# Optimization experiments

Measured on AMD Instinct MI355X. Metric: run time of the kernel, lower is better.

Reference implementation:

```python
import jax, jax.numpy as jnp
import numpy as np

N = 100000          # number of nodes (nums)
E = 1200000         # nnz of the normalized adjacency
D = 64              # embed_size; layer_size = [64, 64, 64]
NODE_DROP = 0.1     # args.node_dropout[0]
MESS_DROP = (0.1, 0.1, 0.1)
EPS = 1e-12         # F.normalize eps


def setup_inputs() -> dict:
    key = jax.random.key(0)
    ks = jax.random.split(key, 10)
    rows = jax.random.randint(ks[0], (E,), 0, N, dtype=jnp.int32)
    cols = jax.random.randint(ks[1], (E,), 0, N, dtype=jnp.int32)
    vals = jax.random.uniform(ks[2], (E,), dtype=jnp.float32)
    emb = jax.random.normal(ks[3], (N, D), dtype=jnp.float32) * 0.1
    W0 = jax.random.normal(ks[4], (D, D), dtype=jnp.float32) * 0.1
    b0 = jax.random.normal(ks[5], (1, D), dtype=jnp.float32) * 0.1
    W1 = jax.random.normal(ks[6], (D, D), dtype=jnp.float32) * 0.1
    b1 = jax.random.normal(ks[7], (1, D), dtype=jnp.float32) * 0.1
    W2 = jax.random.normal(ks[8], (D, D), dtype=jnp.float32) * 0.1
    b2 = jax.random.normal(ks[9], (1, D), dtype=jnp.float32) * 0.1
    return dict(rows=rows, cols=cols, vals=vals, emb=emb,
                W0=W0, b0=b0, W1=W1, b1=b1, W2=W2, b2=b2)


def reference(rows, cols, vals, emb, W0, b0, W1, b1, W2, b2):
    drop_key = jax.random.key(42)
    k_node, k0, k1, k2 = jax.random.split(drop_key, 4)

    # sparse node dropout: zero dropped edge values (== removing nnz), scale survivors
    keep_e = jax.random.bernoulli(k_node, 1.0 - NODE_DROP, (E,))
    a_vals = jnp.where(keep_e, vals / (1.0 - NODE_DROP), 0.0)

    def layer(ego, W, b, rate, k):
        # SpMM: out[r] += a_vals * ego[c]   (COO scatter-add)
        side = jax.ops.segment_sum(a_vals[:, None] * ego[cols], rows, num_segments=N)
        h = side @ W + b
        keep = jax.random.bernoulli(k, 1.0 - rate, h.shape)
        h = jnp.where(keep, h / (1.0 - rate), 0.0)          # mess dropout
        nrm = h / jnp.maximum(jnp.linalg.norm(h, axis=1, keepdims=True), EPS)
        return h, nrm  # ego continues as the (un-normalized) dropped output

    all_embs = [emb]
    ego = emb
    for (W, b, rate, k) in ((W0, b0, MESS_DROP[0], k0),
                            (W1, b1, MESS_DROP[1], k1),
                            (W2, b2, MESS_DROP[2], k2)):
        ego, nrm = layer(ego, W, b, rate, k)
        all_embs.append(nrm)
    return jnp.concatenate(all_embs, axis=1)  # [N, 4*D]
```

## Files before the change

kernel.cpp:

```cpp
#include <hip/hip_runtime.h>
#include <stdint.h>

#define N_NODES 100000
#define DIM 64
#define E_EDGES 1200000
#define RPB 16
#define NB 6250
#define BCAP 264
#define ROW_CAP 40
#define BPB 16

__host__ __device__ __forceinline__ void tf2x32(uint32_t k0, uint32_t k1,
                                                uint32_t c0, uint32_t c1,
                                                uint32_t& o0, uint32_t& o1) {
    uint32_t ks2 = k0 ^ k1 ^ 0x1BD11BDAu;
    uint32_t x0 = c0 + k0, x1 = c1 + k1;
#define TF_RND(r) { x0 += x1; x1 = (x1 << r) | (x1 >> (32 - r)); x1 ^= x0; }
    TF_RND(13) TF_RND(15) TF_RND(26) TF_RND(6)
    x0 += k1;  x1 += ks2 + 1u;
    TF_RND(17) TF_RND(29) TF_RND(16) TF_RND(24)
    x0 += ks2; x1 += k0 + 2u;
    TF_RND(13) TF_RND(15) TF_RND(26) TF_RND(6)
    x0 += k0;  x1 += k1 + 3u;
    TF_RND(17) TF_RND(29) TF_RND(16) TF_RND(24)
    x0 += k1;  x1 += ks2 + 4u;
    TF_RND(13) TF_RND(15) TF_RND(26) TF_RND(6)
    x0 += ks2; x1 += k0 + 5u;
#undef TF_RND
    o0 = x0; o1 = x1;
}

__device__ __forceinline__ bool keep_bit(uint32_t k0, uint32_t k1, uint32_t idx) {
    uint32_t y0, y1;
    tf2x32(k0, k1, 0u, idx, y0, y1);
    return (((y0 ^ y1) >> 9) < 7549747u);
}

__device__ __forceinline__ uint16_t f2bf(float f) {
    uint32_t x = __float_as_uint(f);
    return (uint16_t)((x + 0x7fffu + ((x >> 16) & 1u)) >> 16);
}

__global__ void k_bucket(const int* __restrict__ rows, const int* __restrict__ cols,
                         const float* __restrict__ vals, int* __restrict__ bcnt,
                         int2* __restrict__ bedge, uint32_t k0, uint32_t k1) {
    int i = blockIdx.x * blockDim.x + threadIdx.x;
    int stride = gridDim.x * blockDim.x;
    for (; i < E_EDGES; i += stride) {
        if (keep_bit(k0, k1, (uint32_t)i)) {
            int r = rows[i];
            int b = r >> 4;
            int rl = r & (RPB - 1);
            int pos = atomicAdd(&bcnt[b], 1);
            if (pos < BCAP)
                bedge[(size_t)b * BCAP + pos] =
                    make_int2((rl << 17) | cols[i],
                              __float_as_int(vals[i] * (1.0f / 0.9f)));
        }
    }
}

__global__ __launch_bounds__(256) void k_bin(const int2* __restrict__ bedge,
                                             const int* __restrict__ bcnt,
                                             uint32_t* __restrict__ pairs,
                                             int* __restrict__ cnt) {
    __shared__ uint32_t lp[256 * ROW_CAP];
    __shared__ int lc[256];
    int blk = blockIdx.x, t = threadIdx.x;
    for (int i = t; i < 256 * ROW_CAP / 4; i += 256)
        ((uint4*)lp)[i] = make_uint4(0u, 0u, 0u, 0u);
    lc[t] = 0;
    __syncthreads();
    int b0 = blk * BPB;
    int nb = NB - b0; if (nb > BPB) nb = BPB;
    for (int lb = 0; lb < nb; ++lb) {
        int bb = b0 + lb;
        int ne = bcnt[bb];
        if (ne > BCAP) ne = BCAP;
        const int2* be = bedge + (size_t)bb * BCAP;
        for (int e = t; e < ne; e += 256) {
            int2 en = be[e];
            uint32_t meta = (uint32_t)en.x;
            int rl = (int)(meta >> 17);
            uint32_t col = meta & 0x1FFFFu;
            float v = __int_as_float(en.y);
            int rloc = lb * RPB + rl;
            int pos = atomicAdd(&lc[rloc], 1);
            if (pos < ROW_CAP) {
                uint32_t q = (uint32_t)(v * 16384.0f + 0.5f);
                lp[rloc * ROW_CAP + pos] = (q << 17) | col;
            }
        }
    }
    __syncthreads();
    int nrows = N_NODES - blk * 256;
    if (nrows > 256) nrows = 256;
    int nq = nrows * ROW_CAP / 4;
    uint4* dst = (uint4*)(pairs + (size_t)blk * 256 * ROW_CAP);
    const uint4* src = (const uint4*)lp;
    for (int i = t; i < nq; i += 256) dst[i] = src[i];
    if (t < nrows) cnt[blk * 256 + t] = lc[t];
}

__global__ void k_embcvt(const float* __restrict__ emb, float* __restrict__ out,
                         uint16_t* __restrict__ egoA) {
    int i = blockIdx.x * blockDim.x + threadIdx.x;
    int stride = gridDim.x * blockDim.x;
    const int total = N_NODES * 16;
    for (; i < total; i += stride) {
        int n = i >> 4, q = i & 15;
        float4 v = ((const float4*)emb)[(size_t)n * 16 + q];
        ((float4*)out)[(size_t)n * 64 + q] = v;
        ushort4 bb;
        bb.x = f2bf(v.x); bb.y = f2bf(v.y); bb.z = f2bf(v.z); bb.w = f2bf(v.w);
        ((ushort4*)egoA)[(size_t)n * 16 + q] = bb;
    }
}

#define GATHER_FMA(V, aE, aO)                                              \
    {                                                                      \
        uint32_t c0 = V.x & 0x1FFFFu;  float a0 = (float)(V.x >> 17) * S;  \
        uint32_t c1 = V.y & 0x1FFFFu;  float a1 = (float)(V.y >> 17) * S;  \
        uint32_t c2 = V.z & 0x1FFFFu;  float a2 = (float)(V.z >> 17) * S;  \
        uint32_t c3 = V.w & 0x1FFFFu;  float a3 = (float)(V.w >> 17) * S;  \
        uint32_t u0 = egoU[c0 * 32u + (uint32_t)l2];                       \
        uint32_t u1 = egoU[c1 * 32u + (uint32_t)l2];                       \
        uint32_t u2 = egoU[c2 * 32u + (uint32_t)l2];                       \
        uint32_t u3 = egoU[c3 * 32u + (uint32_t)l2];                       \
        aE = fmaf(a0, __uint_as_float(u0 << 16), aE);                      \
        aO = fmaf(a0, __uint_as_float(u0 & 0xffff0000u), aO);              \
        aE = fmaf(a1, __uint_as_float(u1 << 16), aE);                      \
        aO = fmaf(a1, __uint_as_float(u1 & 0xffff0000u), aO);              \
        aE = fmaf(a2, __uint_as_float(u2 << 16), aE);                      \
        aO = fmaf(a2, __uint_as_float(u2 & 0xffff0000u), aO);              \
        aE = fmaf(a3, __uint_as_float(u3 << 16), aE);                      \
        aO = fmaf(a3, __uint_as_float(u3 & 0xffff0000u), aO);              \
    }

__global__ __launch_bounds__(256, 4) void k_layer(
    const int* __restrict__ cnt, const uint32_t* __restrict__ pairs,
    const uint16_t* __restrict__ ego_in,
    uint16_t* __restrict__ h_out,
    float* __restrict__ out, int coloff,
    const float* __restrict__ W, const float* __restrict__ bias,
    uint32_t k0, uint32_t k1) {
    __shared__ float sS[8][64];
    int t = threadIdx.x;
    int w = t >> 6, lane = t & 63;

    float wreg[64];
#pragma unroll
    for (int k = 0; k < 64; ++k)
        wreg[k] = W[k * 64 + lane];
    float breg = bias[lane];

    const float S = 1.0f / 16384.0f;
    int l2 = lane & 31;
    int hi4 = (lane >> 5) << 2;
    const uint32_t* egoU = (const uint32_t*)ego_in;
    int wid0 = blockIdx.x * 4 + w;
    const int NW = 2048 * 4;
    const int NPAIR = N_NODES / 2;
    for (int nn = wid0; nn < NPAIR; nn += NW) {
        int un0 = __builtin_amdgcn_readfirstlane(nn * 2);
        int un1 = un0 + 1;
        int len0 = (cnt[un0] + 7) & ~7;  if (len0 > ROW_CAP) len0 = ROW_CAP;
        int len1 = (cnt[un1] + 7) & ~7;  if (len1 > ROW_CAP) len1 = ROW_CAP;
        const uint32_t* rowp0 = pairs + (size_t)un0 * ROW_CAP + hi4;
        const uint32_t* rowp1 = pairs + (size_t)un1 * ROW_CAP + hi4;
        float accE0 = 0.f, accO0 = 0.f, accE1 = 0.f, accO1 = 0.f;
        int jmax = len0 > len1 ? len0 : len1;
        for (int j = 0; j < jmax; j += 8) {
            uint4 V0 = (j < len0) ? *reinterpret_cast<const uint4*>(rowp0 + j)
                                  : make_uint4(0u, 0u, 0u, 0u);
            uint4 V1 = (j < len1) ? *reinterpret_cast<const uint4*>(rowp1 + j)
                                  : make_uint4(0u, 0u, 0u, 0u);
            GATHER_FMA(V0, accE0, accO0)
            GATHER_FMA(V1, accE1, accO1)
        }
        accE0 += __shfl_xor(accE0, 32, 64);
        accO0 += __shfl_xor(accO0, 32, 64);
        accE1 += __shfl_xor(accE1, 32, 64);
        accO1 += __shfl_xor(accO1, 32, 64);
        if (lane < 32) {
            reinterpret_cast<float2*>(&sS[2 * w][0])[l2] = make_float2(accE0, accO0);
            reinterpret_cast<float2*>(&sS[2 * w + 1][0])[l2] = make_float2(accE1, accO1);
        }
        float h0 = breg, h1 = breg;
        const float4* s4p0 = reinterpret_cast<const float4*>(&sS[2 * w][0]);
        const float4* s4p1 = reinterpret_cast<const float4*>(&sS[2 * w + 1][0]);
#pragma unroll
        for (int kq = 0; kq < 16; ++kq) {
            float4 s40 = s4p0[kq];
            float4 s41 = s4p1[kq];
            h0 = fmaf(s40.x, wreg[4 * kq + 0], h0);
            h1 = fmaf(s41.x, wreg[4 * kq + 0], h1);
            h0 = fmaf(s40.y, wreg[4 * kq + 1], h0);
            h1 = fmaf(s41.y, wreg[4 * kq + 1], h1);
            h0 = fmaf(s40.z, wreg[4 * kq + 2], h0);
            h1 = fmaf(s41.z, wreg[4 * kq + 2], h1);
            h0 = fmaf(s40.w, wreg[4 * kq + 3], h0);
            h1 = fmaf(s41.w, wreg[4 * kq + 3], h1);
        }
        h0 = keep_bit(k0, k1, (uint32_t)un0 * 64u + (uint32_t)lane) ? h0 * (1.0f / 0.9f) : 0.0f;
        h1 = keep_bit(k0, k1, (uint32_t)un1 * 64u + (uint32_t)lane) ? h1 * (1.0f / 0.9f) : 0.0f;
        float s0 = h0 * h0, s1 = h1 * h1;
#pragma unroll
        for (int o = 32; o > 0; o >>= 1) {
            s0 += __shfl_xor(s0, o, 64);
            s1 += __shfl_xor(s1, o, 64);
        }
        float nv0 = h0 / fmaxf(sqrtf(s0), 1e-12f);
        float nv1 = h1 / fmaxf(sqrtf(s1), 1e-12f);
        if (h_out) {
            h_out[(size_t)un0 * DIM + lane] = f2bf(h0);
            h_out[(size_t)un1 * DIM + lane] = f2bf(h1);
        }
        out[(size_t)un0 * 256 + coloff + lane] = nv0;
        out[(size_t)un1 * 256 + coloff + lane] = nv1;
    }
}

extern "C" void kernel_launch(void* const* d_in, const int* in_sizes, int n_in,
                              void* d_out, int out_size, void* d_ws, size_t ws_size,
                              hipStream_t stream) {
    const int*   rows = (const int*)d_in[0];
    const int*   cols = (const int*)d_in[1];
    const float* vals = (const float*)d_in[2];
    const float* emb  = (const float*)d_in[3];
    const float* Wk[3] = { (const float*)d_in[4], (const float*)d_in[6], (const float*)d_in[8] };
    const float* bk[3] = { (const float*)d_in[5], (const float*)d_in[7], (const float*)d_in[9] };
    float* out = (float*)d_out;

    int*      bcnt  = (int*)d_ws;
    int*      cnt   = bcnt + 8192;
    int2*     bedge = (int2*)((char*)d_ws + 32768 + 400000);
    uint32_t* pairs = (uint32_t*)(bedge + (size_t)NB * BCAP);
    uint16_t* egoA  = (uint16_t*)(pairs + (size_t)N_NODES * ROW_CAP);
    uint16_t* egoB  = egoA + (size_t)N_NODES * DIM;

    uint32_t kn[2], kl[3][2];
    tf2x32(0u, 42u, 0u, 0u, kn[0], kn[1]);
    tf2x32(0u, 42u, 0u, 1u, kl[0][0], kl[0][1]);
    tf2x32(0u, 42u, 0u, 2u, kl[1][0], kl[1][1]);
    tf2x32(0u, 42u, 0u, 3u, kl[2][0], kl[2][1]);

    hipMemsetAsync(bcnt, 0, 8192 * 4, stream);
    k_bucket<<<2048, 256, 0, stream>>>(rows, cols, vals, bcnt, bedge, kn[0], kn[1]);
    k_bin<<<(NB + BPB - 1) / BPB, 256, 0, stream>>>(bedge, bcnt, pairs, cnt);
    k_embcvt<<<2048, 256, 0, stream>>>(emb, out, egoA);

    k_layer<<<2048, 256, 0, stream>>>(cnt, pairs, egoA, egoB, out, 64,
                                      Wk[0], bk[0], kl[0][0], kl[0][1]);
    k_layer<<<2048, 256, 0, stream>>>(cnt, pairs, egoB, egoA, out, 128,
                                      Wk[1], bk[1], kl[1][0], kl[1][1]);
    k_layer<<<2048, 256, 0, stream>>>(cnt, pairs, egoA, nullptr, out, 192,
                                      Wk[2], bk[2], kl[2][0], kl[2][1]);
}
```

Measured before the change: 237.5 us.

## Replicate bucket counters, fuse counter reset into embcvt, process four rows per wave

Bucket counters are replicated 8 ways by block index to reduce atomic contention in k_bucket, and k_bin consumes the replicas with one wave per cell. The memset is folded into k_embcvt, which now runs first. k_layer handles four rows per wave instead of two, giving more gather loads in flight, with launch bounds lowered to 3 blocks per SM. The risks are lower occupancy, per-replica overflow at 64 entries silently dropping edges, and more padded iterations when row lengths differ.

```diff
diff --git a/kernel.cpp b/kernel.cpp
--- a/kernel.cpp
+++ b/kernel.cpp
@@ -4,9 +4,9 @@
 #define N_NODES 100000
 #define DIM 64
 #define E_EDGES 1200000
-#define RPB 16
-#define NB 6250
-#define BCAP 264
+#define NBK 6250
+#define NREP 8
+#define BCAP_R 64
 #define ROW_CAP 40
 #define BPB 16
 
@@ -41,19 +41,37 @@
     return (uint16_t)((x + 0x7fffu + ((x >> 16) & 1u)) >> 16);
 }
 
+__global__ void k_embcvt(const float* __restrict__ emb, float* __restrict__ out,
+                         uint16_t* __restrict__ egoA, int* __restrict__ bcnt) {
+    int gid = blockIdx.x * blockDim.x + threadIdx.x;
+    if (gid < NREP * NBK) bcnt[gid] = 0;
+    int stride = gridDim.x * blockDim.x;
+    const int total = N_NODES * 16;
+    for (int i = gid; i < total; i += stride) {
+        int n = i >> 4, q = i & 15;
+        float4 v = ((const float4*)emb)[(size_t)n * 16 + q];
+        ((float4*)out)[(size_t)n * 64 + q] = v;
+        ushort4 bb;
+        bb.x = f2bf(v.x); bb.y = f2bf(v.y); bb.z = f2bf(v.z); bb.w = f2bf(v.w);
+        ((ushort4*)egoA)[(size_t)n * 16 + q] = bb;
+    }
+}
+
 __global__ void k_bucket(const int* __restrict__ rows, const int* __restrict__ cols,
                          const float* __restrict__ vals, int* __restrict__ bcnt,
                          int2* __restrict__ bedge, uint32_t k0, uint32_t k1) {
+    int rep = blockIdx.x & (NREP - 1);
     int i = blockIdx.x * blockDim.x + threadIdx.x;
     int stride = gridDim.x * blockDim.x;
     for (; i < E_EDGES; i += stride) {
         if (keep_bit(k0, k1, (uint32_t)i)) {
             int r = rows[i];
             int b = r >> 4;
-            int rl = r & (RPB - 1);
-            int pos = atomicAdd(&bcnt[b], 1);
-            if (pos < BCAP)
-                bedge[(size_t)b * BCAP + pos] =
+            int rl = r & 15;
+            int cell = rep * NBK + b;
+            int pos = atomicAdd(&bcnt[cell], 1);
+            if (pos < BCAP_R)
+                bedge[(size_t)cell * BCAP_R + pos] =
                     make_int2((rl << 17) | cols[i],
                               __float_as_int(vals[i] * (1.0f / 0.9f)));
         }
@@ -66,25 +84,30 @@
                                              int* __restrict__ cnt) {
     __shared__ uint32_t lp[256 * ROW_CAP];
     __shared__ int lc[256];
+    __shared__ int lcc[BPB * NREP];
     int blk = blockIdx.x, t = threadIdx.x;
     for (int i = t; i < 256 * ROW_CAP / 4; i += 256)
         ((uint4*)lp)[i] = make_uint4(0u, 0u, 0u, 0u);
     lc[t] = 0;
+    int b0 = blk * BPB;
+    if (t < BPB * NREP) {
+        int lb = t >> 3, rep = t & 7;
+        int ne = bcnt[rep * NBK + b0 + lb];
+        lcc[t] = (ne > BCAP_R) ? BCAP_R : ne;
+    }
     __syncthreads();
-    int b0 = blk * BPB;
-    int nb = NB - b0; if (nb > BPB) nb = BPB;
-    for (int lb = 0; lb < nb; ++lb) {
-        int bb = b0 + lb;
-        int ne = bcnt[bb];
-        if (ne > BCAP) ne = BCAP;
-        const int2* be = bedge + (size_t)bb * BCAP;
-        for (int e = t; e < ne; e += 256) {
-            int2 en = be[e];
+    int e = t & 63, wv = t >> 6;
+    for (int cc = 0; cc < BPB * NREP; cc += 4) {
+        int cell = cc + wv;
+        int lb = cell >> 3, rep = cell & 7;
+        int ne = lcc[cell];
+        if (e < ne) {
+            int2 en = bedge[((size_t)(rep * NBK + b0 + lb)) * BCAP_R + e];
             uint32_t meta = (uint32_t)en.x;
             int rl = (int)(meta >> 17);
             uint32_t col = meta & 0x1FFFFu;
             float v = __int_as_float(en.y);
-            int rloc = lb * RPB + rl;
+            int rloc = lb * 16 + rl;
             int pos = atomicAdd(&lc[rloc], 1);
             if (pos < ROW_CAP) {
                 uint32_t q = (uint32_t)(v * 16384.0f + 0.5f);
@@ -100,21 +123,6 @@
     const uint4* src = (const uint4*)lp;
     for (int i = t; i < nq; i += 256) dst[i] = src[i];
     if (t < nrows) cnt[blk * 256 + t] = lc[t];
-}
-
-__global__ void k_embcvt(const float* __restrict__ emb, float* __restrict__ out,
-                         uint16_t* __restrict__ egoA) {
-    int i = blockIdx.x * blockDim.x + threadIdx.x;
-    int stride = gridDim.x * blockDim.x;
-    const int total = N_NODES * 16;
-    for (; i < total; i += stride) {
-        int n = i >> 4, q = i & 15;
-        float4 v = ((const float4*)emb)[(size_t)n * 16 + q];
-        ((float4*)out)[(size_t)n * 64 + q] = v;
-        ushort4 bb;
-        bb.x = f2bf(v.x); bb.y = f2bf(v.y); bb.z = f2bf(v.z); bb.w = f2bf(v.w);
-        ((ushort4*)egoA)[(size_t)n * 16 + q] = bb;
-    }
 }
 
 #define GATHER_FMA(V, aE, aO)                                              \
@@ -137,14 +145,14 @@
         aO = fmaf(a3, __uint_as_float(u3 & 0xffff0000u), aO);              \
     }
 
-__global__ __launch_bounds__(256, 4) void k_layer(
+__global__ __launch_bounds__(256, 3) void k_layer(
     const int* __restrict__ cnt, const uint32_t* __restrict__ pairs,
     const uint16_t* __restrict__ ego_in,
     uint16_t* __restrict__ h_out,
     float* __restrict__ out, int coloff,
     const float* __restrict__ W, const float* __restrict__ bias,
     uint32_t k0, uint32_t k1) {
-    __shared__ float sS[8][64];
+    __shared__ float sS[16][64];
     int t = threadIdx.x;
     int w = t >> 6, lane = t & 63;
 
@@ -156,68 +164,90 @@
 
     const float S = 1.0f / 16384.0f;
     int l2 = lane & 31;
-    int hi4 = (lane >> 5) << 2;
+    int hiSel = lane >> 5;
+    int hi4 = hiSel << 2;
     const uint32_t* egoU = (const uint32_t*)ego_in;
     int wid0 = blockIdx.x * 4 + w;
     const int NW = 2048 * 4;
-    const int NPAIR = N_NODES / 2;
-    for (int nn = wid0; nn < NPAIR; nn += NW) {
-        int un0 = __builtin_amdgcn_readfirstlane(nn * 2);
-        int un1 = un0 + 1;
-        int len0 = (cnt[un0] + 7) & ~7;  if (len0 > ROW_CAP) len0 = ROW_CAP;
-        int len1 = (cnt[un1] + 7) & ~7;  if (len1 > ROW_CAP) len1 = ROW_CAP;
-        const uint32_t* rowp0 = pairs + (size_t)un0 * ROW_CAP + hi4;
-        const uint32_t* rowp1 = pairs + (size_t)un1 * ROW_CAP + hi4;
-        float accE0 = 0.f, accO0 = 0.f, accE1 = 0.f, accO1 = 0.f;
-        int jmax = len0 > len1 ? len0 : len1;
+    const int NQ = N_NODES / 4;
+    for (int q = wid0; q < NQ; q += NW) {
+        int un = __builtin_amdgcn_readfirstlane(q * 4);
+        int len0 = (cnt[un + 0] + 7) & ~7;  if (len0 > ROW_CAP) len0 = ROW_CAP;
+        int len1 = (cnt[un + 1] + 7) & ~7;  if (len1 > ROW_CAP) len1 = ROW_CAP;
+        int len2 = (cnt[un + 2] + 7) & ~7;  if (len2 > ROW_CAP) len2 = ROW_CAP;
+        int len3 = (cnt[un + 3] + 7) & ~7;  if (len3 > ROW_CAP) len3 = ROW_CAP;
+        const uint32_t* rp = pairs + (size_t)un * ROW_CAP + hi4;
+        float aE0 = 0.f, aO0 = 0.f, aE1 = 0.f, aO1 = 0.f;
+        float aE2 = 0.f, aO2 = 0.f, aE3 = 0.f, aO3 = 0.f;
+        int jmax = len0;
+        if (len1 > jmax) jmax = len1;
+        if (len2 > jmax) jmax = len2;
+        if (len3 > jmax) jmax = len3;
+        const uint4 zed = make_uint4(0u, 0u, 0u, 0u);
         for (int j = 0; j < jmax; j += 8) {
-            uint4 V0 = (j < len0) ? *reinterpret_cast<const uint4*>(rowp0 + j)
-                                  : make_uint4(0u, 0u, 0u, 0u);
-            uint4 V1 = (j < len1) ? *reinterpret_cast<const uint4*>(rowp1 + j)
-                                  : make_uint4(0u, 0u, 0u, 0u);
-            GATHER_FMA(V0, accE0, accO0)
-            GATHER_FMA(V1, accE1, accO1)
-        }
-        accE0 += __shfl_xor(accE0, 32, 64);
-        accO0 += __shfl_xor(accO0, 32, 64);
-        accE1 += __shfl_xor(accE1, 32, 64);
-        accO1 += __shfl_xor(accO1, 32, 64);
-        if (lane < 32) {
-            reinterpret_cast<float2*>(&sS[2 * w][0])[l2] = make_float2(accE0, accO0);
-            reinterpret_cast<float2*>(&sS[2 * w + 1][0])[l2] = make_float2(accE1, accO1);
-        }
-        float h0 = breg, h1 = breg;
-        const float4* s4p0 = reinterpret_cast<const float4*>(&sS[2 * w][0]);
-        const float4* s4p1 = reinterpret_cast<const float4*>(&sS[2 * w + 1][0]);
+            uint4 V0 = (j < len0) ? *reinterpret_cast<const uint4*>(rp + j) : zed;
+            uint4 V1 = (j < len1) ? *reinterpret_cast<const uint4*>(rp + ROW_CAP + j) : zed;
+            uint4 V2 = (j < len2) ? *reinterpret_cast<const uint4*>(rp + 2 * ROW_CAP + j) : zed;
+            uint4 V3 = (j < len3) ? *reinterpret_cast<const uint4*>(rp + 3 * ROW_CAP + j) : zed;
+            GATHER_FMA(V0, aE0, aO0)
+            GATHER_FMA(V1, aE1, aO1)
+            GATHER_FMA(V2, aE2, aO2)
+            GATHER_FMA(V3, aE3, aO3)
+        }
+        aE0 += __shfl_xor(aE0, 32, 64);  aO0 += __shfl_xor(aO0, 32, 64);
+        aE1 += __shfl_xor(aE1, 32, 64);  aO1 += __shfl_xor(aO1, 32, 64);
+        aE2 += __shfl_xor(aE2, 32, 64);  aO2 += __shfl_xor(aO2, 32, 64);
+        aE3 += __shfl_xor(aE3, 32, 64);  aO3 += __shfl_xor(aO3, 32, 64);
+        float2 vA = hiSel ? make_float2(aE2, aO2) : make_float2(aE0, aO0);
+        float2 vB = hiSel ? make_float2(aE3, aO3) : make_float2(aE1, aO1);
+        reinterpret_cast<float2*>(&sS[4 * w + 2 * hiSel][0])[l2] = vA;
+        reinterpret_cast<float2*>(&sS[4 * w + 2 * hiSel + 1][0])[l2] = vB;
+        float h0 = breg, h1 = breg, h2 = breg, h3 = breg;
+        const float4* s0p = reinterpret_cast<const float4*>(&sS[4 * w + 0][0]);
+        const float4* s1p = reinterpret_cast<const float4*>(&sS[4 * w + 1][0]);
+        const float4* s2p = reinterpret_cast<const float4*>(&sS[4 * w + 2][0]);
+        const float4* s3p = reinterpret_cast<const float4*>(&sS[4 * w + 3][0]);
 #pragma unroll
         for (int kq = 0; kq < 16; ++kq) {
-            float4 s40 = s4p0[kq];
-            float4 s41 = s4p1[kq];
-            h0 = fmaf(s40.x, wreg[4 * kq + 0], h0);
-            h1 = fmaf(s41.x, wreg[4 * kq + 0], h1);
-            h0 = fmaf(s40.y, wreg[4 * kq + 1], h0);
-            h1 = fmaf(s41.y, wreg[4 * kq + 1], h1);
-            h0 = fmaf(s40.z, wreg[4 * kq + 2], h0);
-            h1 = fmaf(s41.z, wreg[4 * kq + 2], h1);
-            h0 = fmaf(s40.w, wreg[4 * kq + 3], h0);
-            h1 = fmaf(s41.w, wreg[4 * kq + 3], h1);
-        }
-        h0 = keep_bit(k0, k1, (uint32_t)un0 * 64u + (uint32_t)lane) ? h0 * (1.0f / 0.9f) : 0.0f;
-        h1 = keep_bit(k0, k1, (uint32_t)un1 * 64u + (uint32_t)lane) ? h1 * (1.0f / 0.9f) : 0.0f;
-        float s0 = h0 * h0, s1 = h1 * h1;
+            float4 s0 = s0p[kq], s1 = s1p[kq], s2 = s2p[kq], s3 = s3p[kq];
+            float w0 = wreg[4 * kq + 0], w1 = wreg[4 * kq + 1];
+            float w2 = wreg[4 * kq + 2], w3 = wreg[4 * kq + 3];
+            h0 = fmaf(s0.x, w0, h0); h1 = fmaf(s1.x, w0, h1);
+            h2 = fmaf(s2.x, w0, h2); h3 = fmaf(s3.x, w0, h3);
+            h0 = fmaf(s0.y, w1, h0); h1 = fmaf(s1.y, w1, h1);
+            h2 = fmaf(s2.y, w1, h2); h3 = fmaf(s3.y, w1, h3);
+            h0 = fmaf(s0.z, w2, h0); h1 = fmaf(s1.z, w2, h1);
+            h2 = fmaf(s2.z, w2, h2); h3 = fmaf(s3.z, w2, h3);
+            h0 = fmaf(s0.w, w3, h0); h1 = fmaf(s1.w, w3, h1);
+            h2 = fmaf(s2.w, w3, h2); h3 = fmaf(s3.w, w3, h3);
+        }
+        uint32_t base_idx = (uint32_t)un * 64u + (uint32_t)lane;
+        h0 = keep_bit(k0, k1, base_idx)        ? h0 * (1.0f / 0.9f) : 0.0f;
+        h1 = keep_bit(k0, k1, base_idx + 64u)  ? h1 * (1.0f / 0.9f) : 0.0f;
+        h2 = keep_bit(k0, k1, base_idx + 128u) ? h2 * (1.0f / 0.9f) : 0.0f;
+        h3 = keep_bit(k0, k1, base_idx + 192u) ? h3 * (1.0f / 0.9f) : 0.0f;
+        float s0 = h0 * h0, s1 = h1 * h1, s2 = h2 * h2, s3 = h3 * h3;
 #pragma unroll
         for (int o = 32; o > 0; o >>= 1) {
             s0 += __shfl_xor(s0, o, 64);
             s1 += __shfl_xor(s1, o, 64);
+            s2 += __shfl_xor(s2, o, 64);
+            s3 += __shfl_xor(s3, o, 64);
         }
         float nv0 = h0 / fmaxf(sqrtf(s0), 1e-12f);
         float nv1 = h1 / fmaxf(sqrtf(s1), 1e-12f);
+        float nv2 = h2 / fmaxf(sqrtf(s2), 1e-12f);
+        float nv3 = h3 / fmaxf(sqrtf(s3), 1e-12f);
         if (h_out) {
-            h_out[(size_t)un0 * DIM + lane] = f2bf(h0);
-            h_out[(size_t)un1 * DIM + lane] = f2bf(h1);
-        }
-        out[(size_t)un0 * 256 + coloff + lane] = nv0;
-        out[(size_t)un1 * 256 + coloff + lane] = nv1;
+            h_out[(size_t)(un + 0) * DIM + lane] = f2bf(h0);
+            h_out[(size_t)(un + 1) * DIM + lane] = f2bf(h1);
+            h_out[(size_t)(un + 2) * DIM + lane] = f2bf(h2);
+            h_out[(size_t)(un + 3) * DIM + lane] = f2bf(h3);
+        }
+        out[(size_t)(un + 0) * 256 + coloff + lane] = nv0;
+        out[(size_t)(un + 1) * 256 + coloff + lane] = nv1;
+        out[(size_t)(un + 2) * 256 + coloff + lane] = nv2;
+        out[(size_t)(un + 3) * 256 + coloff + lane] = nv3;
     }
 }
 
@@ -233,9 +263,10 @@
     float* out = (float*)d_out;
 
     int*      bcnt  = (int*)d_ws;
-    int*      cnt   = bcnt + 8192;
-    int2*     bedge = (int2*)((char*)d_ws + 32768 + 400000);
-    uint32_t* pairs = (uint32_t*)(bedge + (size_t)NB * BCAP);
+    int*      cnt   = bcnt + 65536;
+    int2*     bedge = (int2*)(cnt + 100000 + 14);
+    bedge = (int2*)(((uintptr_t)bedge + 511) & ~(uintptr_t)511);
+    uint32_t* pairs = (uint32_t*)(bedge + (size_t)NREP * NBK * BCAP_R);
     uint16_t* egoA  = (uint16_t*)(pairs + (size_t)N_NODES * ROW_CAP);
     uint16_t* egoB  = egoA + (size_t)N_NODES * DIM;
 
@@ -245,10 +276,9 @@
     tf2x32(0u, 42u, 0u, 2u, kl[1][0], kl[1][1]);
     tf2x32(0u, 42u, 0u, 3u, kl[2][0], kl[2][1]);
 
-    hipMemsetAsync(bcnt, 0, 8192 * 4, stream);
+    k_embcvt<<<2048, 256, 0, stream>>>(emb, out, egoA, bcnt);
     k_bucket<<<2048, 256, 0, stream>>>(rows, cols, vals, bcnt, bedge, kn[0], kn[1]);
-    k_bin<<<(NB + BPB - 1) / BPB, 256, 0, stream>>>(bedge, bcnt, pairs, cnt);
-    k_embcvt<<<2048, 256, 0, stream>>>(emb, out, egoA);
+    k_bin<<<(NBK + BPB - 1) / BPB, 256, 0, stream>>>(bedge, bcnt, pairs, cnt);
 
     k_layer<<<2048, 256, 0, stream>>>(cnt, pairs, egoA, egoB, out, 64,
                                       Wk[0], bk[0], kl[0][0], kl[0][1]);
```

Result: slower. 257.5 us (+8.4%).

## Replicate bucket counters by block to cut atomic contention; fold memset into embcvt

Applied to the files above, without the earlier changes.

The COO bucketing now keeps eight replica bucket arrays, one per block-index modulo eight. This spreads the global atomicAdd contention on each bucket counter across replicas, and each replica has a smaller capacity. The binning kernel reads all replicas, one wavefront per cell, to build the per-row lists. The hipMemsetAsync that cleared the counters is removed and the clearing is folded into the embedding-convert kernel, which now runs first. The trade-off is more workspace, many mostly-empty 64-slot cells read in k_bin, and a new risk that a replica cell overflows its 64-entry cap.

```diff
diff --git a/kernel.cpp b/kernel.cpp
--- a/kernel.cpp
+++ b/kernel.cpp
@@ -4,9 +4,9 @@
 #define N_NODES 100000
 #define DIM 64
 #define E_EDGES 1200000
-#define RPB 16
-#define NB 6250
-#define BCAP 264
+#define NBK 6250
+#define NREP 8
+#define BCAP_R 64
 #define ROW_CAP 40
 #define BPB 16
 
@@ -41,19 +41,37 @@
     return (uint16_t)((x + 0x7fffu + ((x >> 16) & 1u)) >> 16);
 }
 
+__global__ void k_embcvt(const float* __restrict__ emb, float* __restrict__ out,
+                         uint16_t* __restrict__ egoA, int* __restrict__ bcnt) {
+    int gid = blockIdx.x * blockDim.x + threadIdx.x;
+    if (gid < NREP * NBK) bcnt[gid] = 0;
+    int stride = gridDim.x * blockDim.x;
+    const int total = N_NODES * 16;
+    for (int i = gid; i < total; i += stride) {
+        int n = i >> 4, q = i & 15;
+        float4 v = ((const float4*)emb)[(size_t)n * 16 + q];
+        ((float4*)out)[(size_t)n * 64 + q] = v;
+        ushort4 bb;
+        bb.x = f2bf(v.x); bb.y = f2bf(v.y); bb.z = f2bf(v.z); bb.w = f2bf(v.w);
+        ((ushort4*)egoA)[(size_t)n * 16 + q] = bb;
+    }
+}
+
 __global__ void k_bucket(const int* __restrict__ rows, const int* __restrict__ cols,
                          const float* __restrict__ vals, int* __restrict__ bcnt,
                          int2* __restrict__ bedge, uint32_t k0, uint32_t k1) {
+    int rep = blockIdx.x & (NREP - 1);
     int i = blockIdx.x * blockDim.x + threadIdx.x;
     int stride = gridDim.x * blockDim.x;
     for (; i < E_EDGES; i += stride) {
         if (keep_bit(k0, k1, (uint32_t)i)) {
             int r = rows[i];
             int b = r >> 4;
-            int rl = r & (RPB - 1);
-            int pos = atomicAdd(&bcnt[b], 1);
-            if (pos < BCAP)
-                bedge[(size_t)b * BCAP + pos] =
+            int rl = r & 15;
+            int cell = rep * NBK + b;
+            int pos = atomicAdd(&bcnt[cell], 1);
+            if (pos < BCAP_R)
+                bedge[(size_t)cell * BCAP_R + pos] =
                     make_int2((rl << 17) | cols[i],
                               __float_as_int(vals[i] * (1.0f / 0.9f)));
         }
@@ -66,25 +84,30 @@
                                              int* __restrict__ cnt) {
     __shared__ uint32_t lp[256 * ROW_CAP];
     __shared__ int lc[256];
+    __shared__ int lcc[BPB * NREP];
     int blk = blockIdx.x, t = threadIdx.x;
     for (int i = t; i < 256 * ROW_CAP / 4; i += 256)
         ((uint4*)lp)[i] = make_uint4(0u, 0u, 0u, 0u);
     lc[t] = 0;
+    int b0 = blk * BPB;
+    if (t < BPB * NREP) {
+        int lb = t >> 3, rep = t & 7;
+        int ne = bcnt[rep * NBK + b0 + lb];
+        lcc[t] = (ne > BCAP_R) ? BCAP_R : ne;
+    }
     __syncthreads();
-    int b0 = blk * BPB;
-    int nb = NB - b0; if (nb > BPB) nb = BPB;
-    for (int lb = 0; lb < nb; ++lb) {
-        int bb = b0 + lb;
-        int ne = bcnt[bb];
-        if (ne > BCAP) ne = BCAP;
-        const int2* be = bedge + (size_t)bb * BCAP;
-        for (int e = t; e < ne; e += 256) {
-            int2 en = be[e];
+    int e = t & 63, wv = t >> 6;
+    for (int cc = 0; cc < BPB * NREP; cc += 4) {
+        int cell = cc + wv;
+        int lb = cell >> 3, rep = cell & 7;
+        int ne = lcc[cell];
+        if (e < ne) {
+            int2 en = bedge[((size_t)(rep * NBK + b0 + lb)) * BCAP_R + e];
             uint32_t meta = (uint32_t)en.x;
             int rl = (int)(meta >> 17);
             uint32_t col = meta & 0x1FFFFu;
             float v = __int_as_float(en.y);
-            int rloc = lb * RPB + rl;
+            int rloc = lb * 16 + rl;
             int pos = atomicAdd(&lc[rloc], 1);
             if (pos < ROW_CAP) {
                 uint32_t q = (uint32_t)(v * 16384.0f + 0.5f);
@@ -100,21 +123,6 @@
     const uint4* src = (const uint4*)lp;
     for (int i = t; i < nq; i += 256) dst[i] = src[i];
     if (t < nrows) cnt[blk * 256 + t] = lc[t];
-}
-
-__global__ void k_embcvt(const float* __restrict__ emb, float* __restrict__ out,
-                         uint16_t* __restrict__ egoA) {
-    int i = blockIdx.x * blockDim.x + threadIdx.x;
-    int stride = gridDim.x * blockDim.x;
-    const int total = N_NODES * 16;
-    for (; i < total; i += stride) {
-        int n = i >> 4, q = i & 15;
-        float4 v = ((const float4*)emb)[(size_t)n * 16 + q];
-        ((float4*)out)[(size_t)n * 64 + q] = v;
-        ushort4 bb;
-        bb.x = f2bf(v.x); bb.y = f2bf(v.y); bb.z = f2bf(v.z); bb.w = f2bf(v.w);
-        ((ushort4*)egoA)[(size_t)n * 16 + q] = bb;
-    }
 }
 
 #define GATHER_FMA(V, aE, aO)                                              \
@@ -233,9 +241,10 @@
     float* out = (float*)d_out;
 
     int*      bcnt  = (int*)d_ws;
-    int*      cnt   = bcnt + 8192;
-    int2*     bedge = (int2*)((char*)d_ws + 32768 + 400000);
-    uint32_t* pairs = (uint32_t*)(bedge + (size_t)NB * BCAP);
+    int*      cnt   = bcnt + 65536;
+    int2*     bedge = (int2*)(cnt + 100000 + 14);
+    bedge = (int2*)(((uintptr_t)bedge + 511) & ~(uintptr_t)511);
+    uint32_t* pairs = (uint32_t*)(bedge + (size_t)NREP * NBK * BCAP_R);
     uint16_t* egoA  = (uint16_t*)(pairs + (size_t)N_NODES * ROW_CAP);
     uint16_t* egoB  = egoA + (size_t)N_NODES * DIM;
 
@@ -245,10 +254,9 @@
     tf2x32(0u, 42u, 0u, 2u, kl[1][0], kl[1][1]);
     tf2x32(0u, 42u, 0u, 3u, kl[2][0], kl[2][1]);
 
-    hipMemsetAsync(bcnt, 0, 8192 * 4, stream);
+    k_embcvt<<<2048, 256, 0, stream>>>(emb, out, egoA, bcnt);
     k_bucket<<<2048, 256, 0, stream>>>(rows, cols, vals, bcnt, bedge, kn[0], kn[1]);
-    k_bin<<<(NB + BPB - 1) / BPB, 256, 0, stream>>>(bedge, bcnt, pairs, cnt);
-    k_embcvt<<<2048, 256, 0, stream>>>(emb, out, egoA);
+    k_bin<<<(NBK + BPB - 1) / BPB, 256, 0, stream>>>(bedge, bcnt, pairs, cnt);
 
     k_layer<<<2048, 256, 0, stream>>>(cnt, pairs, egoA, egoB, out, 64,
                                       Wk[0], bk[0], kl[0][0], kl[0][1]);
```

Result: faster. 231.9 us (-2.3%).
